# Optimization experiments

Hardware: AMD Instinct MI355X
Metric: run time of the kernel (lower is better)

The kernel has to match this reference:

```python
import jax, jax.numpy as jnp
import numpy as np

TOP_K = 8


def setup_inputs() -> dict:
    key = jax.random.key(0)
    ks = jax.random.split(key, 5)
    T, H, I, E = 4096, 2048, 1024, 64
    s = 0.02
    return {
        "x": jax.random.normal(ks[0], (T, H), jnp.float32),
        "gate_w": jax.random.normal(ks[1], (E, H), jnp.float32) * s,
        "gate_b": jax.random.normal(ks[2], (E,), jnp.float32) * s,
        "fc1_w": jax.random.normal(ks[3], (E, 2 * I, H), jnp.float32) * s,
        "fc2_w": jax.random.normal(ks[4], (E, H, I), jnp.float32) * s,
    }


def reference(x, gate_w, gate_b, fc1_w, fc2_w):
    # Router: [T, E] logits, top-k, softmax over selected logits in fp32.
    E = gate_w.shape[0]
    logits = x @ gate_w.T + gate_b
    topk_logits, topk_idx = jax.lax.top_k(logits, TOP_K)
    w = jax.nn.softmax(topk_logits.astype(jnp.float32), axis=-1).astype(x.dtype)
    # Per-token combine weight for each expert: [T, E] (0 if expert not selected).
    comb = (jax.nn.one_hot(topk_idx, E, dtype=x.dtype) * w[..., None]).sum(axis=1)
    # Scan over experts: each step is one dense GEMM-GeGLU-GEMM with masked combine.
    def body(acc, ew):
        W1, W2, c = ew  # W1 [2I, H], W2 [H, I], c [T]
        h_full = x @ W1.T                       # [T, 2I]
        h, g = jnp.split(h_full, 2, axis=-1)
        a = jax.nn.gelu(h, approximate=False) * (g + 1.0)  # custom GeGLU
        y = a @ W2.T                            # [T, H]
        return acc + c[:, None] * y, None

    out0 = jnp.zeros_like(x)
    out, _ = jax.lax.scan(body, out0, (fc1_w, fc2_w, comb.T))
    return out
```

## Files before the change

kernel.cpp:

```cpp
#include <hip/hip_runtime.h>
#include <hip/hip_bf16.h>
#include <cfloat>
#include <math.h>

#define T_TOK 4096
#define H_DIM 2048
#define E_NUM 64
#define I_DIM 1024
#define TOPK  8
#define BM    640
#define BK    64
#define MAXT  128

typedef __attribute__((ext_vector_type(4))) float f32x4;
typedef __attribute__((ext_vector_type(8))) short bf16x8;
typedef __attribute__((ext_vector_type(4))) int   i32x4;

__device__ __forceinline__ unsigned short f2bf(float f) {
    union { float f; unsigned int u; } v; v.f = f;
    unsigned int r = v.u + 0x7FFFu + ((v.u >> 16) & 1u);
    return (unsigned short)(r >> 16);
}
__device__ __forceinline__ unsigned int pack2(float a, float b) {
    return (unsigned int)f2bf(a) | ((unsigned int)f2bf(b) << 16);
}
__device__ __forceinline__ float bf2f(unsigned short u) {
    union { unsigned int u; float f; } v; v.u = (unsigned int)u << 16; return v.f;
}
__device__ __forceinline__ int cvtpk(float lo, float hi) {
    int r; asm("v_cvt_pk_bf16_f32 %0, %1, %2" : "=v"(r) : "v"(lo), "v"(hi)); return r;
}
__device__ __forceinline__ void gload16(const void* g, void* l) {
    __builtin_amdgcn_global_load_lds((const __attribute__((address_space(1))) unsigned int*)g,
                                     (__attribute__((address_space(3))) unsigned int*)l, 16, 0, 0);
}

__global__ __launch_bounds__(256)
void router_kernel(const float* __restrict__ x, const float* __restrict__ gw,
                   const float* __restrict__ gb, unsigned short* __restrict__ xb,
                   int* __restrict__ topk_idx, float* __restrict__ topk_w,
                   int* __restrict__ counts)
{
    const int t = blockIdx.x;
    const int tid = threadIdx.x;
    __shared__ float xs[H_DIM];
    __shared__ float logits[E_NUM];
    const float* xrow = x + (size_t)t * H_DIM;

    #pragma unroll
    for (int i = 0; i < 2; ++i) {
        int c = i * 1024 + tid * 4;
        f32x4 v = *(const f32x4*)(xrow + c);
        *(f32x4*)(xs + c) = v;
        uint2 pk; pk.x = pack2(v.x, v.y); pk.y = pack2(v.z, v.w);
        *(uint2*)(xb + (size_t)t * H_DIM + c) = pk;
    }
    __syncthreads();

    const int wave = tid >> 6, lane = tid & 63;
    for (int ee = 0; ee < 16; ++ee) {
        const int e = wave * 16 + ee;
        const float* g = gw + (size_t)e * H_DIM;
        float p = 0.f;
        #pragma unroll
        for (int i = 0; i < 8; ++i) {
            int c = (i * 64 + lane) * 4;
            f32x4 gv = *(const f32x4*)(g + c);
            f32x4 xv = *(const f32x4*)(xs + c);
            p += gv.x * xv.x + gv.y * xv.y + gv.z * xv.z + gv.w * xv.w;
        }
        #pragma unroll
        for (int s = 32; s > 0; s >>= 1) p += __shfl_xor(p, s, 64);
        if (lane == 0) logits[e] = p + gb[e];
    }
    __syncthreads();

    if (tid < 64) {
        float cur = logits[tid];
        float wv[TOPK]; int wi[TOPK];
        #pragma unroll
        for (int k = 0; k < TOPK; ++k) {
            float bv = cur; int bi = tid;
            #pragma unroll
            for (int s = 32; s > 0; s >>= 1) {
                float ov = __shfl_xor(bv, s, 64);
                int   oi = __shfl_xor(bi, s, 64);
                if (ov > bv || (ov == bv && oi < bi)) { bv = ov; bi = oi; }
            }
            wv[k] = bv; wi[k] = bi;
            if (tid == bi) cur = -FLT_MAX;
        }
        if (tid == 0) {
            float mx = wv[0], sum = 0.f, ex[TOPK];
            #pragma unroll
            for (int k = 0; k < TOPK; ++k) { ex[k] = expf(wv[k] - mx); sum += ex[k]; }
            #pragma unroll
            for (int k = 0; k < TOPK; ++k) {
                topk_idx[t * TOPK + k] = wi[k];
                topk_w[t * TOPK + k]   = ex[k] / sum;
                atomicAdd(&counts[wi[k]], 1);
            }
        }
    }
}

__global__ void scan_kernel(const int* __restrict__ counts, int* __restrict__ offsets,
                            int* __restrict__ cursors, int* __restrict__ tiles,
                            int* __restrict__ ntiles)
{
    if (threadIdx.x == 0) {
        int acc = 0, nt = 0;
        for (int e = 0; e < E_NUM; ++e) {
            offsets[e] = acc; cursors[e] = acc;
            int c = counts[e];
            for (int m = 0; m * BM < c; ++m) tiles[nt++] = (e << 16) | m;
            acc += c;
        }
        *ntiles = nt;
    }
}

__global__ void assign_kernel(const int* __restrict__ topk_idx, const float* __restrict__ topk_w,
                              int* __restrict__ cursors, int* __restrict__ tok_of,
                              int* __restrict__ pos_of)
{
    int i = blockIdx.x * 256 + threadIdx.x;
    if (i >= T_TOK * TOPK) return;
    int e = topk_idx[i];
    int pos = atomicAdd(&cursors[e], 1);
    tok_of[pos] = i >> 3;
    pos_of[i]   = pos;
}

__global__ __launch_bounds__(512, 1)
void gemm1_kernel(const unsigned short* __restrict__ xb, const float* __restrict__ fc1,
                  const int* __restrict__ counts, const int* __restrict__ offsets,
                  const int* __restrict__ tok_of, const int* __restrict__ tiles,
                  const int* __restrict__ ntiles, unsigned short* __restrict__ a_all)
{
    const int ty = blockIdx.y;
    if (ty >= *ntiles) return;
    const int code = tiles[ty];
    const int e = code >> 16, m0 = (code & 0xffff) * BM;
    const int cnt = counts[e], off = offsets[e];
    const int n0 = blockIdx.x * 64;
    const float* W = fc1 + (size_t)e * (size_t)(2 * I_DIM) * H_DIM;

    __shared__ unsigned short sA[BM * BK];
    __shared__ unsigned short sB[128 * BK];
    __shared__ int sTok[BM];

    const int tid = threadIdx.x;
    {
        int r0 = m0 + tid;
        sTok[tid] = tok_of[off + (r0 < cnt ? r0 : cnt - 1)];
        if (tid < BM - 512) {
            int r1 = m0 + 512 + tid;
            sTok[512 + tid] = tok_of[off + (r1 < cnt ? r1 : cnt - 1)];
        }
    }
    __syncthreads();

    const int wid = tid >> 6, lane = tid & 63;
    const int srow = tid >> 3, sch = tid & 7;
    const int sslot = sch ^ (srow & 7);

    const unsigned short* aSrc[10];
    #pragma unroll
    for (int i = 0; i < 10; ++i) {
        int row = srow + 64 * i;
        aSrc[i] = xb + (size_t)sTok[row] * H_DIM + sslot * 8;
    }
    const float* bSrc[2];
    #pragma unroll
    for (int i = 0; i < 2; ++i) {
        int row = srow + 64 * i;
        int wrow = (row < 64) ? (n0 + row) : (I_DIM + n0 + (row - 64));
        bSrc[i] = W + (size_t)wrow * H_DIM + sch * 8;
    }

    f32x4 accH[5][4], accG[5][4];
    #pragma unroll
    for (int m = 0; m < 5; ++m)
        #pragma unroll
        for (int n = 0; n < 4; ++n) {
            accH[m][n] = (f32x4){0.f, 0.f, 0.f, 0.f};
            accG[m][n] = (f32x4){0.f, 0.f, 0.f, 0.f};
        }

    const int wm = wid * 80;
    const int fr = lane & 15;
    const int kg = lane >> 4;

    f32x4 br[4];

    auto issueB = [&](int k0) {
        #pragma unroll
        for (int i = 0; i < 2; ++i) {
            br[2 * i]     = *(const f32x4*)(bSrc[i] + k0);
            br[2 * i + 1] = *(const f32x4*)(bSrc[i] + k0 + 4);
        }
    };
    auto issueA = [&](int k0) {
        #pragma unroll
        for (int i = 0; i < 10; ++i)
            gload16(aSrc[i] + k0, &sA[(64 * i + 8 * wid) * BK]);
    };
    auto writeB = [&]() {
        #pragma unroll
        for (int i = 0; i < 2; ++i) {
            int row = srow + 64 * i;
            i32x4 pk = (i32x4){cvtpk(br[2*i].x,   br[2*i].y),
                               cvtpk(br[2*i].z,   br[2*i].w),
                               cvtpk(br[2*i+1].x, br[2*i+1].y),
                               cvtpk(br[2*i+1].z, br[2*i+1].w)};
            int byte = (row * 128 + sch * 16) ^ ((row & 7) << 4);
            *(i32x4*)((char*)sB + byte) = pk;
        }
    };
    auto compute = [&]() {
        #pragma unroll
        for (int kk = 0; kk < 2; ++kk) {
            bf16x8 af[5], bh[4], bg[4];
            #pragma unroll
            for (int m = 0; m < 5; ++m) {
                int row = wm + m * 16 + fr;
                af[m] = *(const bf16x8*)((const char*)sA +
                        ((row * 128 + kk * 64 + kg * 16) ^ ((row & 7) << 4)));
            }
            #pragma unroll
            for (int n = 0; n < 4; ++n) {
                int rh = n * 16 + fr;
                bh[n] = *(const bf16x8*)((const char*)sB +
                        ((rh * 128 + kk * 64 + kg * 16) ^ ((rh & 7) << 4)));
                int rg = 64 + rh;
                bg[n] = *(const bf16x8*)((const char*)sB +
                        ((rg * 128 + kk * 64 + kg * 16) ^ ((rg & 7) << 4)));
            }
            #pragma unroll
            for (int m = 0; m < 5; ++m)
                #pragma unroll
                for (int n = 0; n < 4; ++n) {
                    accH[m][n] = __builtin_amdgcn_mfma_f32_16x16x32_bf16(af[m], bh[n], accH[m][n], 0, 0, 0);
                    accG[m][n] = __builtin_amdgcn_mfma_f32_16x16x32_bf16(af[m], bg[n], accG[m][n], 0, 0, 0);
                }
        }
    };

    const int NT = H_DIM / BK;
    issueB(0);
    issueA(0);
    __syncthreads();
    writeB();
    __syncthreads();
    for (int t = 0; t < NT; ++t) {
        if (t + 1 < NT) issueB((t + 1) * BK);
        compute();
        __syncthreads();
        if (t + 1 < NT) { issueA((t + 1) * BK); writeB(); }
        __syncthreads();
    }

    #pragma unroll
    for (int m = 0; m < 5; ++m) {
        int rbase = wm + m * 16 + kg * 4;
        #pragma unroll
        for (int r = 0; r < 4; ++r) {
            int gm = m0 + rbase + r;
            if (gm < cnt) {
                size_t rowoff = (size_t)(off + gm) * I_DIM + n0;
                #pragma unroll
                for (int n = 0; n < 4; ++n) {
                    float h = accH[m][n][r];
                    float g = accG[m][n][r];
                    float a = 0.5f * h * (1.f + erff(h * 0.70710678118f)) * (g + 1.f);
                    a_all[rowoff + n * 16 + fr] = f2bf(a);
                }
            }
        }
    }
}

__global__ __launch_bounds__(512, 1)
void gemm2_kernel(const unsigned short* __restrict__ a_all, const float* __restrict__ fc2,
                  const int* __restrict__ counts, const int* __restrict__ offsets,
                  const int* __restrict__ tiles, const int* __restrict__ ntiles,
                  unsigned short* __restrict__ y)
{
    const int ty = blockIdx.y;
    if (ty >= *ntiles) return;
    const int code = tiles[ty];
    const int e = code >> 16, m0 = (code & 0xffff) * BM;
    const int cnt = counts[e], off = offsets[e];
    const int n0 = blockIdx.x * 128;
    const float* W = fc2 + (size_t)e * (size_t)H_DIM * I_DIM;

    __shared__ unsigned short sA[BM * BK];
    __shared__ unsigned short sB[128 * BK];

    const int tid = threadIdx.x;
    const int wid = tid >> 6, lane = tid & 63;
    const int srow = tid >> 3, sch = tid & 7;
    const int sslot = sch ^ (srow & 7);

    const unsigned short* aSrc[10];
    #pragma unroll
    for (int i = 0; i < 10; ++i) {
        int row = srow + 64 * i;
        aSrc[i] = a_all + (size_t)(off + m0 + row) * I_DIM + sslot * 8;
    }
    const float* bSrc[2];
    #pragma unroll
    for (int i = 0; i < 2; ++i) {
        int row = srow + 64 * i;
        bSrc[i] = W + (size_t)(n0 + row) * I_DIM + sch * 8;
    }

    f32x4 acc[5][8];
    #pragma unroll
    for (int m = 0; m < 5; ++m)
        #pragma unroll
        for (int n = 0; n < 8; ++n) acc[m][n] = (f32x4){0.f, 0.f, 0.f, 0.f};

    const int wm = wid * 80;
    const int fr = lane & 15;
    const int kg = lane >> 4;

    f32x4 br[4];

    auto issueB = [&](int k0) {
        #pragma unroll
        for (int i = 0; i < 2; ++i) {
            br[2 * i]     = *(const f32x4*)(bSrc[i] + k0);
            br[2 * i + 1] = *(const f32x4*)(bSrc[i] + k0 + 4);
        }
    };
    auto issueA = [&](int k0) {
        #pragma unroll
        for (int i = 0; i < 10; ++i)
            gload16(aSrc[i] + k0, &sA[(64 * i + 8 * wid) * BK]);
    };
    auto writeB = [&]() {
        #pragma unroll
        for (int i = 0; i < 2; ++i) {
            int row = srow + 64 * i;
            i32x4 pk = (i32x4){cvtpk(br[2*i].x,   br[2*i].y),
                               cvtpk(br[2*i].z,   br[2*i].w),
                               cvtpk(br[2*i+1].x, br[2*i+1].y),
                               cvtpk(br[2*i+1].z, br[2*i+1].w)};
            int byte = (row * 128 + sch * 16) ^ ((row & 7) << 4);
            *(i32x4*)((char*)sB + byte) = pk;
        }
    };
    auto compute = [&]() {
        #pragma unroll
        for (int kk = 0; kk < 2; ++kk) {
            bf16x8 af[5], bfr[8];
            #pragma unroll
            for (int m = 0; m < 5; ++m) {
                int row = wm + m * 16 + fr;
                af[m] = *(const bf16x8*)((const char*)sA +
                        ((row * 128 + kk * 64 + kg * 16) ^ ((row & 7) << 4)));
            }
            #pragma unroll
            for (int n = 0; n < 8; ++n) {
                int row = n * 16 + fr;
                bfr[n] = *(const bf16x8*)((const char*)sB +
                        ((row * 128 + kk * 64 + kg * 16) ^ ((row & 7) << 4)));
            }
            #pragma unroll
            for (int m = 0; m < 5; ++m)
                #pragma unroll
                for (int n = 0; n < 8; ++n)
                    acc[m][n] = __builtin_amdgcn_mfma_f32_16x16x32_bf16(af[m], bfr[n], acc[m][n], 0, 0, 0);
        }
    };

    const int NT = I_DIM / BK;
    issueB(0);
    issueA(0);
    __syncthreads();
    writeB();
    __syncthreads();
    for (int t = 0; t < NT; ++t) {
        if (t + 1 < NT) issueB((t + 1) * BK);
        compute();
        __syncthreads();
        if (t + 1 < NT) { issueA((t + 1) * BK); writeB(); }
        __syncthreads();
    }

    #pragma unroll
    for (int m = 0; m < 5; ++m) {
        int rbase = wm + m * 16 + kg * 4;
        #pragma unroll
        for (int r = 0; r < 4; ++r) {
            int gm = m0 + rbase + r;
            if (gm < cnt) {
                size_t rowoff = (size_t)(off + gm) * H_DIM + n0;
                #pragma unroll
                for (int n = 0; n < 8; ++n)
                    y[rowoff + n * 16 + fr] = f2bf(acc[m][n][r]);
            }
        }
    }
}

__global__ __launch_bounds__(256)
void combine_kernel(const unsigned short* __restrict__ y, const int* __restrict__ pos_of,
                    const float* __restrict__ topk_w, float* __restrict__ out)
{
    const int t = blockIdx.x;
    const int tid = threadIdx.x;
    __shared__ int   sp[TOPK];
    __shared__ float sw[TOPK];
    if (tid < TOPK) {
        sp[tid] = pos_of[t * TOPK + tid];
        sw[tid] = topk_w[t * TOPK + tid];
    }
    __syncthreads();

    const int c0 = tid * 8;
    float acc[8];
    #pragma unroll
    for (int j = 0; j < 8; ++j) acc[j] = 0.f;
    #pragma unroll
    for (int k = 0; k < TOPK; ++k) {
        const float w = sw[k];
        i32x4 v = *(const i32x4*)(y + (size_t)sp[k] * H_DIM + c0);
        const unsigned short* u = (const unsigned short*)&v;
        #pragma unroll
        for (int j = 0; j < 8; ++j) acc[j] += w * bf2f(u[j]);
    }
    float* orow = out + (size_t)t * H_DIM + c0;
    *(f32x4*)orow       = (f32x4){acc[0], acc[1], acc[2], acc[3]};
    *(f32x4*)(orow + 4) = (f32x4){acc[4], acc[5], acc[6], acc[7]};
}

extern "C" void kernel_launch(void* const* d_in, const int* in_sizes, int n_in,
                              void* d_out, int out_size, void* d_ws, size_t ws_size,
                              hipStream_t stream)
{
    const float* x   = (const float*)d_in[0];
    const float* gw  = (const float*)d_in[1];
    const float* gb  = (const float*)d_in[2];
    const float* fc1 = (const float*)d_in[3];
    const float* fc2 = (const float*)d_in[4];
    float* out = (float*)d_out;

    char* ws = (char*)d_ws;
    size_t o = 0;
    auto alloc = [&](size_t b) { void* p = ws + o; o = (o + b + 255) & ~(size_t)255; return p; };
    unsigned short* xb     = (unsigned short*)alloc((size_t)T_TOK * H_DIM * 2);
    int*            tk_idx = (int*)  alloc((size_t)T_TOK * TOPK * 4);
    float*          tk_w   = (float*)alloc((size_t)T_TOK * TOPK * 4);
    int*            counts = (int*)  alloc(E_NUM * 4);
    int*            offs   = (int*)  alloc(E_NUM * 4);
    int*            curs   = (int*)  alloc(E_NUM * 4);
    int*            tiles  = (int*)  alloc(MAXT * 4);
    int*            ntiles = (int*)  alloc(4);
    int*            tok_of = (int*)  alloc((size_t)T_TOK * TOPK * 4);
    int*            pos_of = (int*)  alloc((size_t)T_TOK * TOPK * 4);
    unsigned short* a_all  = (unsigned short*)alloc((size_t)(T_TOK * TOPK + BM) * I_DIM * 2);
    unsigned short* yb     = (unsigned short*)alloc((size_t)(T_TOK * TOPK + BM) * H_DIM * 2);
    (void)ws_size;

    hipMemsetAsync(counts, 0, E_NUM * 4, stream);

    router_kernel<<<T_TOK, 256, 0, stream>>>(x, gw, gb, xb, tk_idx, tk_w, counts);
    scan_kernel<<<1, 64, 0, stream>>>(counts, offs, curs, tiles, ntiles);
    assign_kernel<<<(T_TOK * TOPK + 255) / 256, 256, 0, stream>>>(tk_idx, tk_w, curs, tok_of, pos_of);
    gemm1_kernel<<<dim3(I_DIM / 64, MAXT), 512, 0, stream>>>(xb, fc1, counts, offs, tok_of,
                                                             tiles, ntiles, a_all);
    gemm2_kernel<<<dim3(H_DIM / 128, MAXT), 512, 0, stream>>>(a_all, fc2, counts, offs,
                                                              tiles, ntiles, yb);
    combine_kernel<<<T_TOK, 256, 0, stream>>>(yb, pos_of, tk_w, out);
}
```

Baseline: 1.145 ms.

## Double-buffer LDS tiles with BK=32 and one barrier per k-step in both GEMMs

Both expert GEMM kernels now use two LDS buffers per operand with K-tile 32, so the next tile's A (global_load_lds) and B (fp32 load, convert to bf16) are issued into the spare buffer while the current one is computed. This removes one of the two barriers per iteration and lets global loads overlap MFMA work. The XOR swizzle is rewritten for 64-byte rows, and s_setprio is raised around the MFMA block. In exchange there are twice as many iterations, each with fewer MFMAs to hide latency behind, and barrier overhead per unit of work goes up.

```diff
diff --git a/kernel.cpp b/kernel.cpp
--- a/kernel.cpp
+++ b/kernel.cpp
@@ -9,7 +9,7 @@
 #define I_DIM 1024
 #define TOPK  8
 #define BM    640
-#define BK    64
+#define BK    32
 #define MAXT  128
 
 typedef __attribute__((ext_vector_type(4))) float f32x4;
@@ -34,6 +34,7 @@
     __builtin_amdgcn_global_load_lds((const __attribute__((address_space(1))) unsigned int*)g,
                                      (__attribute__((address_space(3))) unsigned int*)l, 16, 0, 0);
 }
+__device__ __forceinline__ int xr(int row) { return (row & 3) ^ ((row >> 2) & 3); }
 
 __global__ __launch_bounds__(256)
 void router_kernel(const float* __restrict__ x, const float* __restrict__ gw,
@@ -146,8 +147,8 @@
     const int n0 = blockIdx.x * 64;
     const float* W = fc1 + (size_t)e * (size_t)(2 * I_DIM) * H_DIM;
 
-    __shared__ unsigned short sA[BM * BK];
-    __shared__ unsigned short sB[128 * BK];
+    __shared__ unsigned short sA[2][BM * BK];
+    __shared__ unsigned short sB[2][128 * BK];
     __shared__ int sTok[BM];
 
     const int tid = threadIdx.x;
@@ -162,22 +163,17 @@
     __syncthreads();
 
     const int wid = tid >> 6, lane = tid & 63;
-    const int srow = tid >> 3, sch = tid & 7;
-    const int sslot = sch ^ (srow & 7);
-
-    const unsigned short* aSrc[10];
-    #pragma unroll
-    for (int i = 0; i < 10; ++i) {
-        int row = srow + 64 * i;
-        aSrc[i] = xb + (size_t)sTok[row] * H_DIM + sslot * 8;
-    }
-    const float* bSrc[2];
-    #pragma unroll
-    for (int i = 0; i < 2; ++i) {
-        int row = srow + 64 * i;
-        int wrow = (row < 64) ? (n0 + row) : (I_DIM + n0 + (row - 64));
-        bSrc[i] = W + (size_t)wrow * H_DIM + sch * 8;
-    }
+    const int srow = tid >> 2, sch = tid & 3;
+
+    const unsigned short* aSrc[5];
+    #pragma unroll
+    for (int i = 0; i < 5; ++i) {
+        int row = srow + 128 * i;
+        aSrc[i] = xb + (size_t)sTok[row] * H_DIM + (sch ^ xr(row)) * 8;
+    }
+    const float* bSrc = W + (size_t)((srow < 64) ? (n0 + srow) : (I_DIM + n0 + (srow - 64))) * H_DIM
+                        + sch * 8;
+    const int bByte = srow * 64 + ((sch ^ xr(srow)) * 16);
 
     f32x4 accH[5][4], accG[5][4];
     #pragma unroll
@@ -192,73 +188,60 @@
     const int fr = lane & 15;
     const int kg = lane >> 4;
 
-    f32x4 br[4];
+    f32x4 br[2];
 
     auto issueB = [&](int k0) {
-        #pragma unroll
-        for (int i = 0; i < 2; ++i) {
-            br[2 * i]     = *(const f32x4*)(bSrc[i] + k0);
-            br[2 * i + 1] = *(const f32x4*)(bSrc[i] + k0 + 4);
-        }
-    };
-    auto issueA = [&](int k0) {
-        #pragma unroll
-        for (int i = 0; i < 10; ++i)
-            gload16(aSrc[i] + k0, &sA[(64 * i + 8 * wid) * BK]);
-    };
-    auto writeB = [&]() {
-        #pragma unroll
-        for (int i = 0; i < 2; ++i) {
-            int row = srow + 64 * i;
-            i32x4 pk = (i32x4){cvtpk(br[2*i].x,   br[2*i].y),
-                               cvtpk(br[2*i].z,   br[2*i].w),
-                               cvtpk(br[2*i+1].x, br[2*i+1].y),
-                               cvtpk(br[2*i+1].z, br[2*i+1].w)};
-            int byte = (row * 128 + sch * 16) ^ ((row & 7) << 4);
-            *(i32x4*)((char*)sB + byte) = pk;
-        }
-    };
-    auto compute = [&]() {
-        #pragma unroll
-        for (int kk = 0; kk < 2; ++kk) {
-            bf16x8 af[5], bh[4], bg[4];
-            #pragma unroll
-            for (int m = 0; m < 5; ++m) {
-                int row = wm + m * 16 + fr;
-                af[m] = *(const bf16x8*)((const char*)sA +
-                        ((row * 128 + kk * 64 + kg * 16) ^ ((row & 7) << 4)));
-            }
+        br[0] = *(const f32x4*)(bSrc + k0);
+        br[1] = *(const f32x4*)(bSrc + k0 + 4);
+    };
+    auto issueA = [&](int k0, int buf) {
+        #pragma unroll
+        for (int i = 0; i < 5; ++i)
+            gload16(aSrc[i] + k0, &sA[buf][(128 * i + srow) * BK + sch * 8]);
+    };
+    auto writeB = [&](int buf) {
+        i32x4 pk = (i32x4){cvtpk(br[0].x, br[0].y), cvtpk(br[0].z, br[0].w),
+                           cvtpk(br[1].x, br[1].y), cvtpk(br[1].z, br[1].w)};
+        *(i32x4*)((char*)sB[buf] + bByte) = pk;
+    };
+    auto compute = [&](int buf) {
+        bf16x8 af[5], bh[4], bg[4];
+        #pragma unroll
+        for (int m = 0; m < 5; ++m) {
+            int row = wm + m * 16 + fr;
+            af[m] = *(const bf16x8*)((const char*)sA[buf] + row * 64 + ((kg ^ xr(row)) * 16));
+        }
+        #pragma unroll
+        for (int n = 0; n < 4; ++n) {
+            int rh = n * 16 + fr;
+            bh[n] = *(const bf16x8*)((const char*)sB[buf] + rh * 64 + ((kg ^ xr(rh)) * 16));
+            int rg = 64 + rh;
+            bg[n] = *(const bf16x8*)((const char*)sB[buf] + rg * 64 + ((kg ^ xr(rg)) * 16));
+        }
+        __builtin_amdgcn_s_setprio(1);
+        #pragma unroll
+        for (int m = 0; m < 5; ++m)
             #pragma unroll
             for (int n = 0; n < 4; ++n) {
-                int rh = n * 16 + fr;
-                bh[n] = *(const bf16x8*)((const char*)sB +
-                        ((rh * 128 + kk * 64 + kg * 16) ^ ((rh & 7) << 4)));
-                int rg = 64 + rh;
-                bg[n] = *(const bf16x8*)((const char*)sB +
-                        ((rg * 128 + kk * 64 + kg * 16) ^ ((rg & 7) << 4)));
+                accH[m][n] = __builtin_amdgcn_mfma_f32_16x16x32_bf16(af[m], bh[n], accH[m][n], 0, 0, 0);
+                accG[m][n] = __builtin_amdgcn_mfma_f32_16x16x32_bf16(af[m], bg[n], accG[m][n], 0, 0, 0);
             }
-            #pragma unroll
-            for (int m = 0; m < 5; ++m)
-                #pragma unroll
-                for (int n = 0; n < 4; ++n) {
-                    accH[m][n] = __builtin_amdgcn_mfma_f32_16x16x32_bf16(af[m], bh[n], accH[m][n], 0, 0, 0);
-                    accG[m][n] = __builtin_amdgcn_mfma_f32_16x16x32_bf16(af[m], bg[n], accG[m][n], 0, 0, 0);
-                }
-        }
+        __builtin_amdgcn_s_setprio(0);
     };
 
     const int NT = H_DIM / BK;
     issueB(0);
-    issueA(0);
-    __syncthreads();
-    writeB();
-    __syncthreads();
+    issueA(0, 0);
+    writeB(0);
+    __syncthreads();
+    int cur = 0;
     for (int t = 0; t < NT; ++t) {
-        if (t + 1 < NT) issueB((t + 1) * BK);
-        compute();
+        const bool more = (t + 1) < NT;
+        if (more) { issueB((t + 1) * BK); issueA((t + 1) * BK, cur ^ 1); }
+        compute(cur);
+        if (more) writeB(cur ^ 1);
         __syncthreads();
-        if (t + 1 < NT) { issueA((t + 1) * BK); writeB(); }
-        __syncthreads();
+        cur ^= 1;
     }
 
     #pragma unroll
@@ -295,26 +278,21 @@
     const int n0 = blockIdx.x * 128;
     const float* W = fc2 + (size_t)e * (size_t)H_DIM * I_DIM;
 
-    __shared__ unsigned short sA[BM * BK];
-    __shared__ unsigned short sB[128 * BK];
+    __shared__ unsigned short sA[2][BM * BK];
+    __shared__ unsigned short sB[2][128 * BK];
 
     const int tid = threadIdx.x;
     const int wid = tid >> 6, lane = tid & 63;
-    const int srow = tid >> 3, sch = tid & 7;
-    const int sslot = sch ^ (srow & 7);
-
-    const unsigned short* aSrc[10];
-    #pragma unroll
-    for (int i = 0; i < 10; ++i) {
-        int row = srow + 64 * i;
-        aSrc[i] = a_all + (size_t)(off + m0 + row) * I_DIM + sslot * 8;
-    }
-    const float* bSrc[2];
-    #pragma unroll
-    for (int i = 0; i < 2; ++i) {
-        int row = srow + 64 * i;
-        bSrc[i] = W + (size_t)(n0 + row) * I_DIM + sch * 8;
-    }
+    const int srow = tid >> 2, sch = tid & 3;
+
+    const unsigned short* aSrc[5];
+    #pragma unroll
+    for (int i = 0; i < 5; ++i) {
+        int row = srow + 128 * i;
+        aSrc[i] = a_all + (size_t)(off + m0 + row) * I_DIM + (sch ^ xr(row)) * 8;
+    }
+    const float* bSrc = W + (size_t)(n0 + srow) * I_DIM + sch * 8;
+    const int bByte = srow * 64 + ((sch ^ xr(srow)) * 16);
 
     f32x4 acc[5][8];
     #pragma unroll
@@ -326,68 +304,56 @@
     const int fr = lane & 15;
     const int kg = lane >> 4;
 
-    f32x4 br[4];
+    f32x4 br[2];
 
     auto issueB = [&](int k0) {
-        #pragma unroll
-        for (int i = 0; i < 2; ++i) {
-            br[2 * i]     = *(const f32x4*)(bSrc[i] + k0);
-            br[2 * i + 1] = *(const f32x4*)(bSrc[i] + k0 + 4);
-        }
-    };
-    auto issueA = [&](int k0) {
-        #pragma unroll
-        for (int i = 0; i < 10; ++i)
-            gload16(aSrc[i] + k0, &sA[(64 * i + 8 * wid) * BK]);
-    };
-    auto writeB = [&]() {
-        #pragma unroll
-        for (int i = 0; i < 2; ++i) {
-            int row = srow + 64 * i;
-            i32x4 pk = (i32x4){cvtpk(br[2*i].x,   br[2*i].y),
-                               cvtpk(br[2*i].z,   br[2*i].w),
-                               cvtpk(br[2*i+1].x, br[2*i+1].y),
-                               cvtpk(br[2*i+1].z, br[2*i+1].w)};
-            int byte = (row * 128 + sch * 16) ^ ((row & 7) << 4);
-            *(i32x4*)((char*)sB + byte) = pk;
-        }
-    };
-    auto compute = [&]() {
-        #pragma unroll
-        for (int kk = 0; kk < 2; ++kk) {
-            bf16x8 af[5], bfr[8];
+        br[0] = *(const f32x4*)(bSrc + k0);
+        br[1] = *(const f32x4*)(bSrc + k0 + 4);
+    };
+    auto issueA = [&](int k0, int buf) {
+        #pragma unroll
+        for (int i = 0; i < 5; ++i)
+            gload16(aSrc[i] + k0, &sA[buf][(128 * i + srow) * BK + sch * 8]);
+    };
+    auto writeB = [&](int buf) {
+        i32x4 pk = (i32x4){cvtpk(br[0].x, br[0].y), cvtpk(br[0].z, br[0].w),
+                           cvtpk(br[1].x, br[1].y), cvtpk(br[1].z, br[1].w)};
+        *(i32x4*)((char*)sB[buf] + bByte) = pk;
+    };
+    auto compute = [&](int buf) {
+        bf16x8 af[5], bfr[8];
+        #pragma unroll
+        for (int m = 0; m < 5; ++m) {
+            int row = wm + m * 16 + fr;
+            af[m] = *(const bf16x8*)((const char*)sA[buf] + row * 64 + ((kg ^ xr(row)) * 16));
+        }
+        #pragma unroll
+        for (int n = 0; n < 8; ++n) {
+            int row = n * 16 + fr;
+            bfr[n] = *(const bf16x8*)((const char*)sB[buf] + row * 64 + ((kg ^ xr(row)) * 16));
+        }
+        __builtin_amdgcn_s_setprio(1);
+        #pragma unroll
+        for (int m = 0; m < 5; ++m)
             #pragma unroll
-            for (int m = 0; m < 5; ++m) {
-                int row = wm + m * 16 + fr;
-                af[m] = *(const bf16x8*)((const char*)sA +
-                        ((row * 128 + kk * 64 + kg * 16) ^ ((row & 7) << 4)));
-            }
-            #pragma unroll
-            for (int n = 0; n < 8; ++n) {
-                int row = n * 16 + fr;
-                bfr[n] = *(const bf16x8*)((const char*)sB +
-                        ((row * 128 + kk * 64 + kg * 16) ^ ((row & 7) << 4)));
-            }
-            #pragma unroll
-            for (int m = 0; m < 5; ++m)
-                #pragma unroll
-                for (int n = 0; n < 8; ++n)
-                    acc[m][n] = __builtin_amdgcn_mfma_f32_16x16x32_bf16(af[m], bfr[n], acc[m][n], 0, 0, 0);
-        }
+            for (int n = 0; n < 8; ++n)
+                acc[m][n] = __builtin_amdgcn_mfma_f32_16x16x32_bf16(af[m], bfr[n], acc[m][n], 0, 0, 0);
+        __builtin_amdgcn_s_setprio(0);
     };
 
     const int NT = I_DIM / BK;
     issueB(0);
-    issueA(0);
-    __syncthreads();
-    writeB();
-    __syncthreads();
+    issueA(0, 0);
+    writeB(0);
+    __syncthreads();
+    int cur = 0;
     for (int t = 0; t < NT; ++t) {
-        if (t + 1 < NT) issueB((t + 1) * BK);
-        compute();
+        const bool more = (t + 1) < NT;
+        if (more) { issueB((t + 1) * BK); issueA((t + 1) * BK, cur ^ 1); }
+        compute(cur);
+        if (more) writeB(cur ^ 1);
         __syncthreads();
-        if (t + 1 < NT) { issueA((t + 1) * BK); writeB(); }
-        __syncthreads();
+        cur ^= 1;
     }
 
     #pragma unroll
```

Measured after the change: 1.171 ms. 1.02x slower.
